# Optimization experiments

Hardware: AMD Instinct MI355X
Metric: run time of the kernel (lower is better)

## Reference

```python
import jax, jax.numpy as jnp
import numpy as np

GROUPS = 16
KS = 3
EPS = 1e-5  # torch InstanceNorm2d default


def _leaky(x):
    return jnp.where(x > 0, x, 0.1 * x)


def setup_inputs() -> dict:
    key = jax.random.key(0)
    ks = jax.random.split(key, 9)
    B, C, H, W = 8, 256, 128, 128
    R = 512
    s = 0.05
    return {
        "x": jax.random.normal(ks[0], (B, C, H, W), jnp.float32),
        "representation": jax.random.normal(ks[1], (B, R), jnp.float32),
        # SConv.compress_key: Linear(R, C*3*3, bias=False)
        "w_key": jax.random.normal(ks[2], (C * KS * KS, R), jnp.float32) * s,
        # SRAdaIN gamma/beta Linears (R -> C, no bias)
        "w_gamma": jax.random.normal(ks[3], (C, R), jnp.float32) * s,
        "w_beta": jax.random.normal(ks[4], (C, R), jnp.float32) * s,
        # SCM: 1x1 convs R -> R/4 -> C (no bias), PReLU single param init 0.25
        "w_ca1": jax.random.normal(ks[5], (R // 4, R), jnp.float32) * s,
        "prelu_a": jnp.float32(0.25),
        "w_ca2": jax.random.normal(ks[6], (C, R // 4), jnp.float32) * s,
        # ConvLayer: 1x1 conv C -> C with bias
        "w_conv2": jax.random.normal(ks[7], (C, C), jnp.float32) * s,
        "b_conv2": jax.random.normal(ks[8], (C,), jnp.float32) * s,
    }


def reference(x, representation, w_key, w_gamma, w_beta, w_ca1, prelu_a, w_ca2, w_conv2, b_conv2):
    b, c_in, h, w = x.shape
    c_out = w_conv2.shape[0]
    fpg = c_in // GROUPS  # features per group

    # ---- SConv: per-sample dynamic grouped conv (reflection pad, valid conv) ----
    xp = jnp.pad(x, ((0, 0), (0, 0), (1, 1), (1, 1)), mode='reflect')
    # kernel: (b, c_out, 1, 3, 3) then repeat_interleave over in-per-group dim
    kern = _leaky(representation @ w_key.T).reshape(b, c_out, 1, KS, KS)
    kern = jnp.broadcast_to(kern, (b, c_out, fpg, KS, KS))

    def one_conv(xi, ki):
        # xi: (c_in, h+2, w+2); ki: (c_out, fpg, 3, 3)
        return jax.lax.conv_general_dilated(
            xi[None], ki, (1, 1), 'VALID',
            feature_group_count=GROUPS,
            dimension_numbers=('NCHW', 'OIHW', 'NCHW'))[0]

    out = jax.vmap(one_conv)(xp, kern)  # (b, c_out, h, w)

    # ---- SRAdaIN: instance norm (biased var) + learned affine from rep ----
    mean = out.mean(axis=(2, 3), keepdims=True)
    var = out.var(axis=(2, 3), keepdims=True)
    gamma = _leaky(representation @ w_gamma.T)[:, :, None, None]
    beta = _leaky(representation @ w_beta.T)[:, :, None, None]
    out = (out - mean) * jax.lax.rsqrt(var + EPS) * gamma + beta
    out = jax.nn.relu(out)

    # ---- SCM: channel attention gating of the residual ----
    hmid = representation @ w_ca1.T
    hmid = jnp.where(hmid > 0, hmid, prelu_a * hmid)  # PReLU
    att = jax.nn.sigmoid(hmid @ w_ca2.T)[:, :, None, None]  # (b, c_out, 1, 1)
    out = out + x * att

    # ---- ConvLayer: 1x1 conv with bias (pad=0) ----
    out = jnp.einsum('bchw,oc->bohw', out, w_conv2) + b_conv2[None, :, None, None]
    return out
```

## Files before the change

kernel.cpp:

```cpp
#include <hip/hip_runtime.h>
#include <hip/hip_bf16.h>

#define NB 8
#define NC 256
#define NH 128
#define NW 128
#define NR 512
#define NGROUPS 16
#define HP 130
#define NPIX (NH*NW)

#define OFF_KERN  0
#define OFF_GAMMA 18432
#define OFF_BETA  20480
#define OFF_ATT   22528
#define OFF_A     24576
#define OFF_B2    26624
#define OFF_HMID  28672
#define OFF_P     29696
#define OFF_GP    94208
#define OFF_APACK 2257408
#define OFF_PART  2322944

typedef __attribute__((ext_vector_type(8))) short bf16x8;
typedef __attribute__((ext_vector_type(4))) float f32x4;

__device__ __forceinline__ float leakyf(float v) { return v > 0.f ? v : 0.1f * v; }

__device__ __forceinline__ unsigned short f2bf(float f) {
    unsigned u = __float_as_uint(f);
    unsigned r = (u + 0x7FFFu + ((u >> 16) & 1u)) >> 16;
    return (unsigned short)r;
}
__device__ __forceinline__ float bf2f(unsigned short s) {
    return __uint_as_float(((unsigned)s) << 16);
}

__global__ __launch_bounds__(256) void k_params(
    const float* __restrict__ rep, const float* __restrict__ w_key,
    const float* __restrict__ w_gamma, const float* __restrict__ w_beta,
    const float* __restrict__ w_ca1, const float* __restrict__ prelu_a,
    float* __restrict__ ws)
{
    __shared__ float rep_s[NR];
    const int b = blockIdx.y, t = threadIdx.x;
    rep_s[t]       = rep[b*NR + t];
    rep_s[t + 256] = rep[b*NR + t + 256];
    __syncthreads();

    const int r = blockIdx.x * 64 + (t >> 2);
    const int part = t & 3;
    const float* wrow;
    if (r < 2304)      wrow = w_key   + (size_t)r * NR;
    else if (r < 2560) wrow = w_gamma + (size_t)(r - 2304) * NR;
    else if (r < 2816) wrow = w_beta  + (size_t)(r - 2560) * NR;
    else               wrow = w_ca1   + (size_t)(r - 2816) * NR;

    const float4* w4 = (const float4*)wrow + part*32;
    const float4* r4 = (const float4*)rep_s + part*32;
    float acc = 0.f;
    #pragma unroll
    for (int i = 0; i < 32; i++) {
        float4 a = r4[i], w = w4[i];
        acc += a.x*w.x + a.y*w.y + a.z*w.z + a.w*w.w;
    }
    acc += __shfl_xor(acc, 1, 64);
    acc += __shfl_xor(acc, 2, 64);

    if (part == 0) {
        if (r < 2816) {
            const float v = leakyf(acc);
            if (r < 2304)      ws[OFF_KERN  + b*NC*9 + r]        = v;
            else if (r < 2560) ws[OFF_GAMMA + b*NC + r - 2304]   = v;
            else               ws[OFF_BETA  + b*NC + r - 2560]   = v;
        } else {
            const float pa = prelu_a[0];
            ws[OFF_HMID + b*128 + r - 2816] = acc > 0.f ? acc : pa * acc;
        }
    }
}

__global__ __launch_bounds__(256) void k_pack(
    const float* __restrict__ W, float* __restrict__ ws)
{
    const int idx = blockIdx.x * 256 + threadIdx.x;
    const int j    = idx & 7;
    const int lane = (idx >> 3) & 63;
    const int mt   = (idx >> 9) & 15;
    const int ks   = idx >> 13;
    const int m = mt*16 + (lane & 15);
    const int k = ks*32 + (lane >> 4)*8 + j;
    unsigned short* ap = (unsigned short*)(ws + OFF_APACK);
    ap[((ks*16 + mt)*64 + lane)*8 + j] = f2bf(W[m*NC + k]);
}

__global__ __launch_bounds__(256) void k_gsum(
    const float* __restrict__ x, float* __restrict__ ws)
{
    const int t = threadIdx.x;
    const int l = t & 31;
    const int r = t >> 5;
    const int bid = blockIdx.x;
    const int rg = bid % 17;
    const int bg = bid / 17;
    const int yy = rg*8 + r;
    if (yy >= HP) return;
    int sy = yy - 1; if (sy < 0) sy = -sy; if (sy > NH-1) sy = 2*(NH-1) - sy;
    const float* xbase = x + (size_t)bg * 16 * NPIX + (size_t)sy * NW + l*4;
    float4 s = make_float4(0.f, 0.f, 0.f, 0.f);
    #pragma unroll
    for (int k = 0; k < 16; k++) {
        const float4 v = *(const float4*)(xbase + (size_t)k * NPIX);
        s.x += v.x; s.y += v.y; s.z += v.z; s.w += v.w;
    }
    float* gp = ws + OFF_GP + ((size_t)bg * HP + yy) * HP;
    gp[1 + l*4] = s.x;
    gp[2 + l*4] = s.y;
    gp[3 + l*4] = s.z;
    gp[4 + l*4] = s.w;
    if (l == 0)  gp[0]   = s.y;
    if (l == 31) gp[129] = s.z;
}

__global__ __launch_bounds__(256) void k_stats(float* __restrict__ ws)
{
    const int g = blockIdx.x, b = blockIdx.y, chunk = blockIdx.z, t = threadIdx.x;
    __shared__ float kern_s[16*9];
    __shared__ float red[256*32];
    if (t < 144) kern_s[t] = ws[OFF_KERN + (b*NC + g*16)*9 + t];
    __syncthreads();

    float s[16], q[16];
    #pragma unroll
    for (int i = 0; i < 16; i++) { s[i] = 0.f; q[i] = 0.f; }

    const float* gp = ws + OFF_GP + (size_t)(b*16 + g) * HP * HP;
    const int p0b = chunk * 4096;
    for (int pi = 0; pi < 16; pi++) {
        const int p = p0b + pi*256 + t;
        const int y = p >> 7, xc = p & 127;
        const float* pa = gp + y*HP + xc;
        const float p0 = pa[0],    p1 = pa[1],      p2 = pa[2];
        const float p3 = pa[HP],   p4 = pa[HP+1],   p5 = pa[HP+2];
        const float p6 = pa[2*HP], p7 = pa[2*HP+1], p8 = pa[2*HP+2];
        #pragma unroll
        for (int ch = 0; ch < 16; ch++) {
            const float* k9 = kern_s + ch*9;
            float v = k9[0]*p0 + k9[1]*p1 + k9[2]*p2
                    + k9[3]*p3 + k9[4]*p4 + k9[5]*p5
                    + k9[6]*p6 + k9[7]*p7 + k9[8]*p8;
            s[ch] += v; q[ch] += v*v;
        }
    }
    #pragma unroll
    for (int ch = 0; ch < 16; ch++) { red[t*32 + ch] = s[ch]; red[t*32 + 16 + ch] = q[ch]; }
    for (int st = 128; st >= 1; st >>= 1) {
        __syncthreads();
        if (t < st) {
            #pragma unroll
            for (int v = 0; v < 32; v++) red[t*32 + v] += red[(t+st)*32 + v];
        }
    }
    __syncthreads();
    if (t < 32) {
        ws[OFF_PART + (size_t)((b*16 + g)*4 + chunk)*32 + t] = red[t];
    }
}

__global__ __launch_bounds__(256) void k_fin(
    const float* __restrict__ w_ca2, float* __restrict__ ws)
{
    __shared__ float hm_s[128];
    const int b = blockIdx.x, c = threadIdx.x;
    if (c < 128) hm_s[c] = ws[OFF_HMID + b*128 + c];
    float* P = ws + OFF_P + ((size_t)(b*NC + c) << 4);
    {
        const int g = c >> 4, ch = c & 15;
        const float* part = ws + OFF_PART + (size_t)(b*16 + g)*4*32;
        float S = 0.f, Q = 0.f;
        #pragma unroll
        for (int k = 0; k < 4; k++) { S += part[k*32 + ch]; Q += part[k*32 + 16 + ch]; }
        const float mean = S * (1.f/16384.f);
        const float var  = Q * (1.f/16384.f) - mean*mean;
        const float inv  = rsqrtf(var + 1e-5f);
        const float ga = ws[OFF_GAMMA + b*NC + c];
        const float be = ws[OFF_BETA  + b*NC + c];
        const float a  = ga * inv;
        #pragma unroll
        for (int k = 0; k < 9; k++) P[k] = ws[OFF_KERN + (b*NC + c)*9 + k];
        P[9]  = a;
        P[10] = be - mean * a;
    }
    __syncthreads();
    {
        const float4* w4 = (const float4*)(w_ca2 + c*128);
        const float4* h4 = (const float4*)hm_s;
        float acc = 0.f;
        #pragma unroll
        for (int i = 0; i < 32; i++) {
            float4 a = h4[i], w = w4[i];
            acc += a.x*w.x + a.y*w.y + a.z*w.z + a.w*w.w;
        }
        P[11] = 1.f / (1.f + expf(-acc));
    }
}

__global__ __launch_bounds__(256) void k_main(
    const float* __restrict__ x, const float* __restrict__ ws,
    const float* __restrict__ bias, float* __restrict__ out)
{
    __shared__ unsigned short z_t[32*256];
    __shared__ float4 P_s[800];
    __shared__ float bias_s[NC];

    const int t = threadIdx.x;
    const int wave = t >> 6, lane = t & 63;
    const int x0 = blockIdx.x * 32, y = blockIdx.y, b = blockIdx.z;

    bias_s[t] = bias[t];

    {
        const float4* Pg = (const float4*)(ws + OFF_P + ((size_t)(b*NC) << 4));
        #pragma unroll
        for (int i = 0; i < 3; i++) {
            const int idx = t + i*256;
            const int c = idx / 3, k = idx - c*3;
            P_s[c*3 + k + (c >> 3)] = Pg[c*4 + k];
        }
    }

    char* zb = (char*)z_t;

    const int pxq = lane & 7;
    const int chs = (lane >> 3) & 7;
    const int cw8 = wave*64 + chs*8;
    const int g   = cw8 >> 4;
    const int px0g = x0 + pxq*4;
    const float* gpB = ws + OFF_GP + (size_t)b * 16 * HP * HP;
    const unsigned short* ap = (const unsigned short*)(ws + OFF_APACK);
    const float* xB = x + (size_t)(b*NC + cw8) * NPIX + (size_t)y * NW + px0g;

    float gp6[3][6];
    {
        const float* gpr = gpB + ((size_t)g * HP + y) * HP + px0g;
        #pragma unroll
        for (int r = 0; r < 3; r++) {
            const float2 a0 = *(const float2*)(gpr + r*HP);
            const float2 a1 = *(const float2*)(gpr + r*HP + 2);
            const float2 a2 = *(const float2*)(gpr + r*HP + 4);
            gp6[r][0] = a0.x; gp6[r][1] = a0.y;
            gp6[r][2] = a1.x; gp6[r][3] = a1.y;
            gp6[r][4] = a2.x; gp6[r][5] = a2.y;
        }
    }
    float4 xq[8];
    #pragma unroll
    for (int j = 0; j < 8; j++) xq[j] = *(const float4*)(xB + (size_t)j * NPIX);

    __syncthreads();

    bf16x8 zp[4];
    const int base_f4 = cw8*3 + (cw8 >> 3);
    #pragma unroll
    for (int j = 0; j < 8; j++) {
        const float4 q0 = P_s[base_f4 + j*3 + 0];
        const float4 q1 = P_s[base_f4 + j*3 + 1];
        const float4 q2 = P_s[base_f4 + j*3 + 2];
        const float xj[4] = {xq[j].x, xq[j].y, xq[j].z, xq[j].w};
        #pragma unroll
        for (int i = 0; i < 4; i++) {
            const float conv =
                  gp6[0][i]*q0.x + gp6[0][i+1]*q0.y + gp6[0][i+2]*q0.z
                + gp6[1][i]*q0.w + gp6[1][i+1]*q1.x + gp6[1][i+2]*q1.y
                + gp6[2][i]*q1.z + gp6[2][i+1]*q1.w + gp6[2][i+2]*q2.x;
            const float z = fmaxf(fmaf(q2.y, conv, q2.z), 0.f) + xj[i] * q2.w;
            zp[i][j] = (short)f2bf(z);
        }
    }
    #pragma unroll
    for (int i = 0; i < 4; i++) {
        const int px = pxq*4 + i;
        *(bf16x8*)(zb + px*512 + ((cw8*2) ^ ((px & 31) << 4))) = zp[i];
    }
    __syncthreads();

    f32x4 acc[4][2];
    #pragma unroll
    for (int mi = 0; mi < 4; mi++) {
        acc[mi][0] = (f32x4){0.f, 0.f, 0.f, 0.f};
        acc[mi][1] = (f32x4){0.f, 0.f, 0.f, 0.f};
    }

    #pragma unroll
    for (int ks = 0; ks < 8; ks++) {
        bf16x8 bfr[2];
        #pragma unroll
        for (int ni = 0; ni < 2; ni++) {
            const int pxc = ni*16 + (lane & 15);
            bfr[ni] = *(const bf16x8*)(zb + pxc*512 + ((ks*64 + (lane >> 4)*16) ^ ((pxc & 31) << 4)));
        }
        #pragma unroll
        for (int mi = 0; mi < 4; mi++) {
            const bf16x8 afr = *(const bf16x8*)(ap + ((size_t)((ks*16 + wave*4 + mi))*64 + lane)*8);
            #pragma unroll
            for (int ni = 0; ni < 2; ni++)
                acc[mi][ni] = __builtin_amdgcn_mfma_f32_16x16x32_bf16(afr, bfr[ni], acc[mi][ni], 0, 0, 0);
        }
    }

    #pragma unroll
    for (int mi = 0; mi < 4; mi++) {
        const int o_base = wave*64 + mi*16 + (lane >> 4)*4;
        #pragma unroll
        for (int ni = 0; ni < 2; ni++) {
            const int px = x0 + ni*16 + (lane & 15);
            #pragma unroll
            for (int r = 0; r < 4; r++) {
                const int o = o_base + r;
                out[((size_t)(b*NC + o) * NH + y) * NW + px] = acc[mi][ni][r] + bias_s[o];
            }
        }
    }
}

extern "C" void kernel_launch(void* const* d_in, const int* in_sizes, int n_in,
                              void* d_out, int out_size, void* d_ws, size_t ws_size,
                              hipStream_t stream) {
    const float* x       = (const float*)d_in[0];
    const float* rep     = (const float*)d_in[1];
    const float* w_key   = (const float*)d_in[2];
    const float* w_gamma = (const float*)d_in[3];
    const float* w_beta  = (const float*)d_in[4];
    const float* w_ca1   = (const float*)d_in[5];
    const float* prelu_a = (const float*)d_in[6];
    const float* w_ca2   = (const float*)d_in[7];
    const float* w_conv2 = (const float*)d_in[8];
    const float* b_conv2 = (const float*)d_in[9];
    float* out = (float*)d_out;
    float* ws  = (float*)d_ws;

    k_params<<<dim3(46, NB), 256, 0, stream>>>(rep, w_key, w_gamma, w_beta, w_ca1, prelu_a, ws);
    k_pack<<<256, 256, 0, stream>>>(w_conv2, ws);
    k_gsum<<<NB*NGROUPS*17, 256, 0, stream>>>(x, ws);
    k_stats<<<dim3(NGROUPS, NB, 4), 256, 0, stream>>>(ws);
    k_fin<<<NB, 256, 0, stream>>>(w_ca2, ws);
    k_main<<<dim3(4, NH, NB), 256, 0, stream>>>(x, ws, b_conv2, out);
}
```

Before: 124.6 us.

## Merge prep kernels into one launch, pack bf16 pairs, fold bias into accumulator

Combines the parameter GEMV, weight-packing and group-sum kernels into one launch whose work is chosen by block index, removing two launches and the gaps between them. In the main kernel, pairs of channel values are converted to bf16 with one packed convert instruction instead of scalar rounding. The conv bias now initialises the MFMA accumulators rather than being added at store time. The fused kernel's blocks run independent work with very different lengths, and the __syncthreads sits inside a block-uniform branch.

```diff
diff --git a/kernel.cpp b/kernel.cpp
--- a/kernel.cpp
+++ b/kernel.cpp
@@ -36,90 +36,87 @@
     return __uint_as_float(((unsigned)s) << 16);
 }
 
-__global__ __launch_bounds__(256) void k_params(
+__global__ __launch_bounds__(256) void k_prep(
     const float* __restrict__ rep, const float* __restrict__ w_key,
     const float* __restrict__ w_gamma, const float* __restrict__ w_beta,
     const float* __restrict__ w_ca1, const float* __restrict__ prelu_a,
+    const float* __restrict__ W, const float* __restrict__ x,
     float* __restrict__ ws)
 {
     __shared__ float rep_s[NR];
-    const int b = blockIdx.y, t = threadIdx.x;
-    rep_s[t]       = rep[b*NR + t];
-    rep_s[t + 256] = rep[b*NR + t + 256];
-    __syncthreads();
-
-    const int r = blockIdx.x * 64 + (t >> 2);
-    const int part = t & 3;
-    const float* wrow;
-    if (r < 2304)      wrow = w_key   + (size_t)r * NR;
-    else if (r < 2560) wrow = w_gamma + (size_t)(r - 2304) * NR;
-    else if (r < 2816) wrow = w_beta  + (size_t)(r - 2560) * NR;
-    else               wrow = w_ca1   + (size_t)(r - 2816) * NR;
-
-    const float4* w4 = (const float4*)wrow + part*32;
-    const float4* r4 = (const float4*)rep_s + part*32;
-    float acc = 0.f;
-    #pragma unroll
-    for (int i = 0; i < 32; i++) {
-        float4 a = r4[i], w = w4[i];
-        acc += a.x*w.x + a.y*w.y + a.z*w.z + a.w*w.w;
-    }
-    acc += __shfl_xor(acc, 1, 64);
-    acc += __shfl_xor(acc, 2, 64);
-
-    if (part == 0) {
-        if (r < 2816) {
-            const float v = leakyf(acc);
-            if (r < 2304)      ws[OFF_KERN  + b*NC*9 + r]        = v;
-            else if (r < 2560) ws[OFF_GAMMA + b*NC + r - 2304]   = v;
-            else               ws[OFF_BETA  + b*NC + r - 2560]   = v;
-        } else {
-            const float pa = prelu_a[0];
-            ws[OFF_HMID + b*128 + r - 2816] = acc > 0.f ? acc : pa * acc;
-        }
-    }
-}
-
-__global__ __launch_bounds__(256) void k_pack(
-    const float* __restrict__ W, float* __restrict__ ws)
-{
-    const int idx = blockIdx.x * 256 + threadIdx.x;
-    const int j    = idx & 7;
-    const int lane = (idx >> 3) & 63;
-    const int mt   = (idx >> 9) & 15;
-    const int ks   = idx >> 13;
-    const int m = mt*16 + (lane & 15);
-    const int k = ks*32 + (lane >> 4)*8 + j;
-    unsigned short* ap = (unsigned short*)(ws + OFF_APACK);
-    ap[((ks*16 + mt)*64 + lane)*8 + j] = f2bf(W[m*NC + k]);
-}
-
-__global__ __launch_bounds__(256) void k_gsum(
-    const float* __restrict__ x, float* __restrict__ ws)
-{
+    const int id = blockIdx.x;
     const int t = threadIdx.x;
-    const int l = t & 31;
-    const int r = t >> 5;
-    const int bid = blockIdx.x;
-    const int rg = bid % 17;
-    const int bg = bid / 17;
-    const int yy = rg*8 + r;
-    if (yy >= HP) return;
-    int sy = yy - 1; if (sy < 0) sy = -sy; if (sy > NH-1) sy = 2*(NH-1) - sy;
-    const float* xbase = x + (size_t)bg * 16 * NPIX + (size_t)sy * NW + l*4;
-    float4 s = make_float4(0.f, 0.f, 0.f, 0.f);
-    #pragma unroll
-    for (int k = 0; k < 16; k++) {
-        const float4 v = *(const float4*)(xbase + (size_t)k * NPIX);
-        s.x += v.x; s.y += v.y; s.z += v.z; s.w += v.w;
-    }
-    float* gp = ws + OFF_GP + ((size_t)bg * HP + yy) * HP;
-    gp[1 + l*4] = s.x;
-    gp[2 + l*4] = s.y;
-    gp[3 + l*4] = s.z;
-    gp[4 + l*4] = s.w;
-    if (l == 0)  gp[0]   = s.y;
-    if (l == 31) gp[129] = s.z;
+
+    if (id < 368) {
+        const int b = id / 46, rblk = id % 46;
+        rep_s[t]       = rep[b*NR + t];
+        rep_s[t + 256] = rep[b*NR + t + 256];
+        __syncthreads();
+
+        const int r = rblk * 64 + (t >> 2);
+        const int part = t & 3;
+        const float* wrow;
+        if (r < 2304)      wrow = w_key   + (size_t)r * NR;
+        else if (r < 2560) wrow = w_gamma + (size_t)(r - 2304) * NR;
+        else if (r < 2816) wrow = w_beta  + (size_t)(r - 2560) * NR;
+        else               wrow = w_ca1   + (size_t)(r - 2816) * NR;
+
+        const float4* w4 = (const float4*)wrow + part*32;
+        const float4* r4 = (const float4*)rep_s + part*32;
+        float acc = 0.f;
+        #pragma unroll
+        for (int i = 0; i < 32; i++) {
+            float4 a = r4[i], w = w4[i];
+            acc += a.x*w.x + a.y*w.y + a.z*w.z + a.w*w.w;
+        }
+        acc += __shfl_xor(acc, 1, 64);
+        acc += __shfl_xor(acc, 2, 64);
+
+        if (part == 0) {
+            if (r < 2816) {
+                const float v = leakyf(acc);
+                if (r < 2304)      ws[OFF_KERN  + b*NC*9 + r]        = v;
+                else if (r < 2560) ws[OFF_GAMMA + b*NC + r - 2304]   = v;
+                else               ws[OFF_BETA  + b*NC + r - 2560]   = v;
+            } else {
+                const float pa = prelu_a[0];
+                ws[OFF_HMID + b*128 + r - 2816] = acc > 0.f ? acc : pa * acc;
+            }
+        }
+    } else if (id < 624) {
+        const int idx = (id - 368) * 256 + t;
+        const int j    = idx & 7;
+        const int lane = (idx >> 3) & 63;
+        const int mt   = (idx >> 9) & 15;
+        const int ks   = idx >> 13;
+        const int m = mt*16 + (lane & 15);
+        const int k = ks*32 + (lane >> 4)*8 + j;
+        unsigned short* ap = (unsigned short*)(ws + OFF_APACK);
+        ap[((ks*16 + mt)*64 + lane)*8 + j] = f2bf(W[m*NC + k]);
+    } else {
+        const int bid = id - 624;
+        const int l = t & 31;
+        const int r = t >> 5;
+        const int rg = bid % 17;
+        const int bg = bid / 17;
+        const int yy = rg*8 + r;
+        if (yy >= HP) return;
+        int sy = yy - 1; if (sy < 0) sy = -sy; if (sy > NH-1) sy = 2*(NH-1) - sy;
+        const float* xbase = x + (size_t)bg * 16 * NPIX + (size_t)sy * NW + l*4;
+        float4 s = make_float4(0.f, 0.f, 0.f, 0.f);
+        #pragma unroll
+        for (int k = 0; k < 16; k++) {
+            const float4 v = *(const float4*)(xbase + (size_t)k * NPIX);
+            s.x += v.x; s.y += v.y; s.z += v.z; s.w += v.w;
+        }
+        float* gp = ws + OFF_GP + ((size_t)bg * HP + yy) * HP;
+        gp[1 + l*4] = s.x;
+        gp[2 + l*4] = s.y;
+        gp[3 + l*4] = s.z;
+        gp[4 + l*4] = s.w;
+        if (l == 0)  gp[0]   = s.y;
+        if (l == 31) gp[129] = s.z;
+    }
 }
 
 __global__ __launch_bounds__(256) void k_stats(float* __restrict__ ws)
@@ -259,36 +256,50 @@
 
     __syncthreads();
 
-    bf16x8 zp[4];
+    unsigned int wm[4][4];
     const int base_f4 = cw8*3 + (cw8 >> 3);
     #pragma unroll
-    for (int j = 0; j < 8; j++) {
-        const float4 q0 = P_s[base_f4 + j*3 + 0];
-        const float4 q1 = P_s[base_f4 + j*3 + 1];
-        const float4 q2 = P_s[base_f4 + j*3 + 2];
-        const float xj[4] = {xq[j].x, xq[j].y, xq[j].z, xq[j].w};
+    for (int jp = 0; jp < 4; jp++) {
+        const float4 qa0 = P_s[base_f4 + (2*jp)*3 + 0];
+        const float4 qa1 = P_s[base_f4 + (2*jp)*3 + 1];
+        const float4 qa2 = P_s[base_f4 + (2*jp)*3 + 2];
+        const float4 qb0 = P_s[base_f4 + (2*jp+1)*3 + 0];
+        const float4 qb1 = P_s[base_f4 + (2*jp+1)*3 + 1];
+        const float4 qb2 = P_s[base_f4 + (2*jp+1)*3 + 2];
+        const float xja[4] = {xq[2*jp].x,   xq[2*jp].y,   xq[2*jp].z,   xq[2*jp].w};
+        const float xjb[4] = {xq[2*jp+1].x, xq[2*jp+1].y, xq[2*jp+1].z, xq[2*jp+1].w};
         #pragma unroll
         for (int i = 0; i < 4; i++) {
-            const float conv =
-                  gp6[0][i]*q0.x + gp6[0][i+1]*q0.y + gp6[0][i+2]*q0.z
-                + gp6[1][i]*q0.w + gp6[1][i+1]*q1.x + gp6[1][i+2]*q1.y
-                + gp6[2][i]*q1.z + gp6[2][i+1]*q1.w + gp6[2][i+2]*q2.x;
-            const float z = fmaxf(fmaf(q2.y, conv, q2.z), 0.f) + xj[i] * q2.w;
-            zp[i][j] = (short)f2bf(z);
+            const float cva =
+                  gp6[0][i]*qa0.x + gp6[0][i+1]*qa0.y + gp6[0][i+2]*qa0.z
+                + gp6[1][i]*qa0.w + gp6[1][i+1]*qa1.x + gp6[1][i+2]*qa1.y
+                + gp6[2][i]*qa1.z + gp6[2][i+1]*qa1.w + gp6[2][i+2]*qa2.x;
+            const float za = fmaxf(fmaf(qa2.y, cva, qa2.z), 0.f) + xja[i] * qa2.w;
+            const float cvb =
+                  gp6[0][i]*qb0.x + gp6[0][i+1]*qb0.y + gp6[0][i+2]*qb0.z
+                + gp6[1][i]*qb0.w + gp6[1][i+1]*qb1.x + gp6[1][i+2]*qb1.y
+                + gp6[2][i]*qb1.z + gp6[2][i+1]*qb1.w + gp6[2][i+2]*qb2.x;
+            const float zbv = fmaxf(fmaf(qb2.y, cvb, qb2.z), 0.f) + xjb[i] * qb2.w;
+            unsigned int w;
+            asm("v_cvt_pk_bf16_f32 %0, %1, %2" : "=v"(w) : "v"(za), "v"(zbv));
+            wm[i][jp] = w;
         }
     }
     #pragma unroll
     for (int i = 0; i < 4; i++) {
         const int px = pxq*4 + i;
-        *(bf16x8*)(zb + px*512 + ((cw8*2) ^ ((px & 31) << 4))) = zp[i];
+        *(uint4*)(zb + px*512 + ((cw8*2) ^ ((px & 31) << 4))) =
+            make_uint4(wm[i][0], wm[i][1], wm[i][2], wm[i][3]);
     }
     __syncthreads();
 
     f32x4 acc[4][2];
     #pragma unroll
     for (int mi = 0; mi < 4; mi++) {
-        acc[mi][0] = (f32x4){0.f, 0.f, 0.f, 0.f};
-        acc[mi][1] = (f32x4){0.f, 0.f, 0.f, 0.f};
+        const int o_base = wave*64 + mi*16 + (lane >> 4)*4;
+        const f32x4 binit = *(const f32x4*)(&bias_s[o_base]);
+        acc[mi][0] = binit;
+        acc[mi][1] = binit;
     }
 
     #pragma unroll
@@ -317,7 +328,7 @@
             #pragma unroll
             for (int r = 0; r < 4; r++) {
                 const int o = o_base + r;
-                out[((size_t)(b*NC + o) * NH + y) * NW + px] = acc[mi][ni][r] + bias_s[o];
+                out[((size_t)(b*NC + o) * NH + y) * NW + px] = acc[mi][ni][r];
             }
         }
     }
@@ -339,9 +350,7 @@
     float* out = (float*)d_out;
     float* ws  = (float*)d_ws;
 
-    k_params<<<dim3(46, NB), 256, 0, stream>>>(rep, w_key, w_gamma, w_beta, w_ca1, prelu_a, ws);
-    k_pack<<<256, 256, 0, stream>>>(w_conv2, ws);
-    k_gsum<<<NB*NGROUPS*17, 256, 0, stream>>>(x, ws);
+    k_prep<<<2800, 256, 0, stream>>>(rep, w_key, w_gamma, w_beta, w_ca1, prelu_a, w_conv2, x, ws);
     k_stats<<<dim3(NGROUPS, NB, 4), 256, 0, stream>>>(ws);
     k_fin<<<NB, 256, 0, stream>>>(w_ca2, ws);
     k_main<<<dim3(4, NH, NB), 256, 0, stream>>>(x, ws, b_conv2, out);
```

Result: faster. 114.0 us (median of 2 runs) (-8.5%).
